# Optimization experiments

Hardware: AMD Instinct MI355X
Metric: run time of the kernel (lower is better)

## Reference

```python
import jax, jax.numpy as jnp
import numpy as np

TOPK = 0.1
LAYER_ID = 2
EPS_COS = 1e-8
EPS_NORM = 1e-12


def setup_inputs() -> dict:
    key = jax.random.key(0)
    k1, k2, k3, k4 = jax.random.split(key, 4)
    B, T, D, H, S, L = 32, 512, 512, 8, 196, 3
    fore_rep_encoded = jax.random.normal(k1, (B, D), dtype=jnp.float32)
    target_embed = jax.random.normal(k2, (B, T, D), dtype=jnp.float32)
    align_attns = jax.random.uniform(k3, (L, B, H, T, S), dtype=jnp.float32)
    targets = jax.random.randint(k4, (B, T + 1), 0, 5000, dtype=jnp.int64)
    return {
        "fore_rep_encoded": fore_rep_encoded,
        "target_embed": target_embed,
        "align_attns": align_attns,
        "targets": targets,
    }


def _normalize(cams):
    # CAM min-max normalization over last dim
    cams = cams - jnp.min(cams, axis=-1, keepdims=True)
    cams_max = jnp.maximum(jnp.max(cams, axis=-1, keepdims=True), EPS_NORM)
    return cams / cams_max


def reference(fore_rep_encoded, target_embed, align_attns, targets):
    B, T, D = target_embed.shape
    tgt = targets[:, :-1]                       # [B, T]
    seq_mask = tgt > 0
    seq_mask = seq_mask.at[:, 0].set(True)      # first position always valid

    attns = jnp.mean(align_attns[LAYER_ID], axis=1)   # [B, T, S] head-averaged

    # cosine similarity along feature dim (torch CosineSimilarity, eps=1e-8)
    x = target_embed                            # [B, T, D]
    y = fore_rep_encoded[:, None, :]            # [B, 1, D]
    num = jnp.sum(x * y, axis=2)                # [B, T]
    xn = jnp.maximum(jnp.sqrt(jnp.sum(x * x, axis=2)), EPS_COS)
    yn = jnp.maximum(jnp.sqrt(jnp.sum(y * y, axis=2)), EPS_COS)
    weights = num / (xn * yn)                   # [B, T]

    weights = jnp.where(seq_mask, weights, -1.0)
    k = int(TOPK * T)
    _, idxs = jax.lax.top_k(weights, k)          # [B, k], sorted descending

    attns = jax.nn.relu(weights[:, :, None] * attns)  # [B, T, S]

    seq_len = jnp.sum(seq_mask, axis=1)          # [B]
    # per-sample true top-k count: ceil(seq_len * topk), clipped to k
    m = jnp.minimum(
        jnp.ceil(seq_len.astype(jnp.float32) * TOPK).astype(jnp.int32), k
    )                                            # [B]

    sel = jnp.take_along_axis(attns, idxs[:, :, None], axis=1)  # [B, k, S]
    valid = (jnp.arange(k)[None, :] < m[:, None])[:, :, None]   # [B, k, 1]
    # masked mean over the per-sample variable-length top-k segment
    total = jnp.sum(jnp.where(valid, sel, 0.0), axis=1) / m[:, None].astype(sel.dtype)
    total_attn = _normalize(total)               # [B, S]
    return total_attn
```

## Files before the change

kernel.cpp:

```cpp
#include <hip/hip_runtime.h>
#include <math.h>

#define B 32
#define T 512
#define D 512
#define H 8
#define S 196
#define K_TOP 51
#define NCHUNK 8
#define LAYER_ID 2

__global__ __launch_bounds__(256) void k_weights(const float* __restrict__ fore,
                                                 const float* __restrict__ te,
                                                 float* __restrict__ weights) {
    int row  = (blockIdx.x * blockDim.x + threadIdx.x) >> 6;
    int lane = threadIdx.x & 63;
    if (row >= B * T) return;
    int b = row >> 9;
    const float4* xp = (const float4*)(te + (size_t)row * D);
    const float4* yp = (const float4*)(fore + (size_t)b * D);
    float4 x0 = xp[lane], x1 = xp[lane + 64];
    float4 y0 = yp[lane], y1 = yp[lane + 64];
    float xy = x0.x*y0.x + x0.y*y0.y + x0.z*y0.z + x0.w*y0.w
             + x1.x*y1.x + x1.y*y1.y + x1.z*y1.z + x1.w*y1.w;
    float xx = x0.x*x0.x + x0.y*x0.y + x0.z*x0.z + x0.w*x0.w
             + x1.x*x1.x + x1.y*x1.y + x1.z*x1.z + x1.w*x1.w;
    float yy = y0.x*y0.x + y0.y*y0.y + y0.z*y0.z + y0.w*y0.w
             + y1.x*y1.x + y1.y*y1.y + y1.z*y1.z + y1.w*y1.w;
    #pragma unroll
    for (int off = 32; off; off >>= 1) {
        xy += __shfl_xor(xy, off);
        xx += __shfl_xor(xx, off);
        yy += __shfl_xor(yy, off);
    }
    if (lane == 0) {
        float xn = fmaxf(sqrtf(xx), 1e-8f);
        float yn = fmaxf(sqrtf(yy), 1e-8f);
        weights[row] = xy / (xn * yn);
    }
}

__global__ __launch_bounds__(512) void k_select(const int* __restrict__ targets,
                                                const float* __restrict__ weights,
                                                int* __restrict__ m_arr,
                                                int* __restrict__ sel_idx,
                                                float* __restrict__ sel_w,
                                                float* __restrict__ totals) {
    int b = blockIdx.x;
    int t = threadIdx.x;
    __shared__ float wsh[T];
    __shared__ int cnt, cnt2, mm;
    if (t == 0) { cnt = 0; cnt2 = 0; }
    __syncthreads();

    int tv = targets[b * (T + 1) + t];
    bool mask = (t == 0) || (tv > 0);
    float w = weights[b * T + t];
    w = mask ? w : -1.0f;
    wsh[t] = w;

    unsigned long long bal = __ballot(mask);
    if ((t & 63) == 0) atomicAdd(&cnt, __popcll(bal));
    __syncthreads();

    if (t == 0) {
        int m = (int)ceilf((float)cnt * 0.1f);
        mm = m < K_TOP ? m : K_TOP;
        m_arr[b] = mm;
    }
    if (t < S) totals[b * S + t] = 0.0f;
    __syncthreads();

    float wt = w;
    int rank = 0;
    for (int j = 0; j < T; ++j) {
        float wj = wsh[j];
        rank += (wj > wt) || (wj == wt && j < t);
    }
    if (rank < mm) {
        int pos = atomicAdd(&cnt2, 1);
        sel_idx[b * 64 + pos] = t;
        sel_w [b * 64 + pos] = wt;
    }
}

__global__ __launch_bounds__(256) void k_accum(const float* __restrict__ align,
                                               const int* __restrict__ m_arr,
                                               const int* __restrict__ sel_idx,
                                               const float* __restrict__ sel_w,
                                               float* __restrict__ totals) {
    int b = blockIdx.y;
    int chunk = blockIdx.x;
    int s = threadIdx.x;
    if (s >= S) return;
    int m = m_arr[b];
    const float* base = align + ((size_t)(LAYER_ID * B + b)) * H * T * S;
    float acc = 0.0f;
    for (int i = chunk; i < m; i += NCHUNK) {
        int   t = sel_idx[b * 64 + i];
        float w = sel_w [b * 64 + i];
        const float* p = base + (size_t)t * S + s;
        float sum = 0.0f;
        #pragma unroll
        for (int h = 0; h < H; ++h) sum += p[(size_t)h * T * S];
        float v = w * (sum * (1.0f / H));
        acc += fmaxf(v, 0.0f);
    }
    atomicAdd(&totals[b * S + s], acc);
}

__global__ __launch_bounds__(256) void k_norm(const float* __restrict__ totals,
                                              const int* __restrict__ m_arr,
                                              float* __restrict__ out) {
    int b = blockIdx.x;
    int s = threadIdx.x;
    __shared__ float smin[256], smax[256];
    float m = (float)m_arr[b];
    float v = (s < S) ? totals[b * S + s] / m : 0.0f;
    smin[s] = (s < S) ? v : 3.0e38f;
    smax[s] = (s < S) ? v : -3.0e38f;
    __syncthreads();
    #pragma unroll
    for (int off = 128; off; off >>= 1) {
        if (s < off) {
            smin[s] = fminf(smin[s], smin[s + off]);
            smax[s] = fmaxf(smax[s], smax[s + off]);
        }
        __syncthreads();
    }
    if (s < S) {
        float mn = smin[0], mx = smax[0];
        out[b * S + s] = (v - mn) / fmaxf(mx - mn, 1e-12f);
    }
}

extern "C" void kernel_launch(void* const* d_in, const int* in_sizes, int n_in,
                              void* d_out, int out_size, void* d_ws, size_t ws_size,
                              hipStream_t stream) {
    const float* fore    = (const float*)d_in[0];
    const float* te      = (const float*)d_in[1];
    const float* align   = (const float*)d_in[2];
    const int*   targets = (const int*)d_in[3];
    float* out = (float*)d_out;

    float* weights = (float*)d_ws;
    int*   m_arr   = (int*)(weights + B * T);
    int*   sel_idx = m_arr + B;
    float* sel_w   = (float*)(sel_idx + B * 64);
    float* totals  = sel_w + B * 64;

    k_weights<<<dim3((B * T) / 4), 256, 0, stream>>>(fore, te, weights);
    k_select <<<dim3(B), 512, 0, stream>>>(targets, weights, m_arr, sel_idx, sel_w, totals);
    k_accum  <<<dim3(NCHUNK, B), 256, 0, stream>>>(align, m_arr, sel_idx, sel_w, totals);
    k_norm   <<<dim3(B), 256, 0, stream>>>(totals, m_arr, out);
}
```

Before: 389.7 us.

## Replace atomic totals with per-chunk partials and double-up select work per thread

k_accum now writes one partial sum per chunk instead of doing an atomicAdd into totals, and k_norm adds up the chunk partials. This removes the zeroing of totals from k_select and avoids atomic contention. The chunk count goes from 8 to 16 to spread the gathered align reads over more blocks. k_select now runs 256 threads, each ranking two positions with float4 reads from LDS, which halves the shared-memory loads per comparison. The cost is more partial traffic in k_norm and fewer threads in the select kernel.

```diff
diff --git a/kernel.cpp b/kernel.cpp
--- a/kernel.cpp
+++ b/kernel.cpp
@@ -7,7 +7,7 @@
 #define H 8
 #define S 196
 #define K_TOP 51
-#define NCHUNK 8
+#define NCHUNK 16
 #define LAYER_ID 2
 
 __global__ __launch_bounds__(256) void k_weights(const float* __restrict__ fore,
@@ -40,47 +40,64 @@
     }
 }
 
-__global__ __launch_bounds__(512) void k_select(const int* __restrict__ targets,
+__global__ __launch_bounds__(256) void k_select(const int* __restrict__ targets,
                                                 const float* __restrict__ weights,
                                                 int* __restrict__ m_arr,
                                                 int* __restrict__ sel_idx,
-                                                float* __restrict__ sel_w,
-                                                float* __restrict__ totals) {
+                                                float* __restrict__ sel_w) {
     int b = blockIdx.x;
-    int t = threadIdx.x;
+    int tid = threadIdx.x;
     __shared__ float wsh[T];
     __shared__ int cnt, cnt2, mm;
-    if (t == 0) { cnt = 0; cnt2 = 0; }
+    if (tid == 0) { cnt = 0; cnt2 = 0; }
     __syncthreads();
 
-    int tv = targets[b * (T + 1) + t];
-    bool mask = (t == 0) || (tv > 0);
-    float w = weights[b * T + t];
-    w = mask ? w : -1.0f;
-    wsh[t] = w;
+    int t0 = tid, t1 = tid + 256;
+    int tv0 = targets[b * (T + 1) + t0];
+    int tv1 = targets[b * (T + 1) + t1];
+    bool mk0 = (t0 == 0) || (tv0 > 0);
+    bool mk1 = (tv1 > 0);
+    float w0 = weights[b * T + t0]; w0 = mk0 ? w0 : -1.0f;
+    float w1 = weights[b * T + t1]; w1 = mk1 ? w1 : -1.0f;
+    wsh[t0] = w0;
+    wsh[t1] = w1;
 
-    unsigned long long bal = __ballot(mask);
-    if ((t & 63) == 0) atomicAdd(&cnt, __popcll(bal));
+    unsigned long long bal0 = __ballot(mk0);
+    unsigned long long bal1 = __ballot(mk1);
+    if ((tid & 63) == 0) atomicAdd(&cnt, __popcll(bal0) + __popcll(bal1));
     __syncthreads();
 
-    if (t == 0) {
+    if (tid == 0) {
         int m = (int)ceilf((float)cnt * 0.1f);
         mm = m < K_TOP ? m : K_TOP;
         m_arr[b] = mm;
     }
-    if (t < S) totals[b * S + t] = 0.0f;
     __syncthreads();
 
-    float wt = w;
-    int rank = 0;
-    for (int j = 0; j < T; ++j) {
-        float wj = wsh[j];
-        rank += (wj > wt) || (wj == wt && j < t);
+    int r0 = 0, r1 = 0;
+    const float4* w4 = (const float4*)wsh;
+    for (int j4 = 0; j4 < T / 4; ++j4) {
+        float4 v = w4[j4];
+        int j = j4 * 4;
+        r0 += (v.x > w0) || (v.x == w0 && (j + 0) < t0);
+        r0 += (v.y > w0) || (v.y == w0 && (j + 1) < t0);
+        r0 += (v.z > w0) || (v.z == w0 && (j + 2) < t0);
+        r0 += (v.w > w0) || (v.w == w0 && (j + 3) < t0);
+        r1 += (v.x > w1) || (v.x == w1 && (j + 0) < t1);
+        r1 += (v.y > w1) || (v.y == w1 && (j + 1) < t1);
+        r1 += (v.z > w1) || (v.z == w1 && (j + 2) < t1);
+        r1 += (v.w > w1) || (v.w == w1 && (j + 3) < t1);
     }
-    if (rank < mm) {
+    int lmm = mm;
+    if (r0 < lmm) {
         int pos = atomicAdd(&cnt2, 1);
-        sel_idx[b * 64 + pos] = t;
-        sel_w [b * 64 + pos] = wt;
+        sel_idx[b * 64 + pos] = t0;
+        sel_w [b * 64 + pos] = w0;
+    }
+    if (r1 < lmm) {
+        int pos = atomicAdd(&cnt2, 1);
+        sel_idx[b * 64 + pos] = t1;
+        sel_w [b * 64 + pos] = w1;
     }
 }
 
@@ -88,7 +105,7 @@
                                                const int* __restrict__ m_arr,
                                                const int* __restrict__ sel_idx,
                                                const float* __restrict__ sel_w,
-                                               float* __restrict__ totals) {
+                                               float* __restrict__ partials) {
     int b = blockIdx.y;
     int chunk = blockIdx.x;
     int s = threadIdx.x;
@@ -106,17 +123,24 @@
         float v = w * (sum * (1.0f / H));
         acc += fmaxf(v, 0.0f);
     }
-    atomicAdd(&totals[b * S + s], acc);
+    partials[((size_t)b * NCHUNK + chunk) * S + s] = acc;
 }
 
-__global__ __launch_bounds__(256) void k_norm(const float* __restrict__ totals,
+__global__ __launch_bounds__(256) void k_norm(const float* __restrict__ partials,
                                               const int* __restrict__ m_arr,
                                               float* __restrict__ out) {
     int b = blockIdx.x;
     int s = threadIdx.x;
     __shared__ float smin[256], smax[256];
     float m = (float)m_arr[b];
-    float v = (s < S) ? totals[b * S + s] / m : 0.0f;
+    float v = 0.0f;
+    if (s < S) {
+        float tot = 0.0f;
+        #pragma unroll
+        for (int c = 0; c < NCHUNK; ++c)
+            tot += partials[((size_t)b * NCHUNK + c) * S + s];
+        v = tot / m;
+    }
     smin[s] = (s < S) ? v : 3.0e38f;
     smax[s] = (s < S) ? v : -3.0e38f;
     __syncthreads();
@@ -143,14 +167,14 @@
     const int*   targets = (const int*)d_in[3];
     float* out = (float*)d_out;
 
-    float* weights = (float*)d_ws;
-    int*   m_arr   = (int*)(weights + B * T);
-    int*   sel_idx = m_arr + B;
-    float* sel_w   = (float*)(sel_idx + B * 64);
-    float* totals  = sel_w + B * 64;
+    float* weights  = (float*)d_ws;
+    int*   m_arr    = (int*)(weights + B * T);
+    int*   sel_idx  = m_arr + B;
+    float* sel_w    = (float*)(sel_idx + B * 64);
+    float* partials = sel_w + B * 64;
 
     k_weights<<<dim3((B * T) / 4), 256, 0, stream>>>(fore, te, weights);
-    k_select <<<dim3(B), 512, 0, stream>>>(targets, weights, m_arr, sel_idx, sel_w, totals);
-    k_accum  <<<dim3(NCHUNK, B), 256, 0, stream>>>(align, m_arr, sel_idx, sel_w, totals);
-    k_norm   <<<dim3(B), 256, 0, stream>>>(totals, m_arr, out);
+    k_select <<<dim3(B), 256, 0, stream>>>(targets, weights, m_arr, sel_idx, sel_w);
+    k_accum  <<<dim3(NCHUNK, B), 256, 0, stream>>>(align, m_arr, sel_idx, sel_w, partials);
+    k_norm   <<<dim3(B), 256, 0, stream>>>(partials, m_arr, out);
 }
```

Result: no change. 389.2 us (-0.1%).
